# Optimization experiments

Measured on AMD Instinct MI355X. Metric: run time of the kernel, lower is better.

## Reference

```python
import jax, jax.numpy as jnp
import numpy as np

N = 100000      # num_nodes
E = 1_600_000   # edges (avg degree 16)
D_IN = 128
D_H = 128
D_OUT = 128


def setup_inputs() -> dict:
    key = jax.random.key(0)
    ks = jax.random.split(key, 11)
    x = jax.random.normal(ks[0], (N, D_IN), dtype=jnp.float32)
    edge_index = jax.random.randint(ks[1], (2, E), 0, N, dtype=jnp.int32)
    s_in = 1.0 / np.sqrt(D_IN)
    s_h = 1.0 / np.sqrt(D_H)
    return {
        "x": x,
        "edge_index": edge_index,
        "W_neigh1": jax.random.uniform(ks[2], (D_H, D_IN), jnp.float32, -s_in, s_in),
        "b_neigh1": jax.random.uniform(ks[3], (D_H,), jnp.float32, -s_in, s_in),
        "W_self1": jax.random.uniform(ks[4], (D_H, D_IN), jnp.float32, -s_in, s_in),
        "b_self1": jax.random.uniform(ks[5], (D_H,), jnp.float32, -s_in, s_in),
        "W_neigh2": jax.random.uniform(ks[6], (D_OUT, D_H), jnp.float32, -s_h, s_h),
        "b_neigh2": jax.random.uniform(ks[7], (D_OUT,), jnp.float32, -s_h, s_h),
        "W_self2": jax.random.uniform(ks[8], (D_OUT, D_H), jnp.float32, -s_h, s_h),
        "b_self2": jax.random.uniform(ks[9], (D_OUT,), jnp.float32, -s_h, s_h),
    }


def reference(x, edge_index, W_neigh1, b_neigh1, W_self1, b_self1,
              W_neigh2, b_neigh2, W_self2, b_self2):
    src, dst = edge_index[0], edge_index[1]
    n = x.shape[0]
    # row-normalized adjacency: deg over dst (row index), clamped to >= 1
    deg = jax.ops.segment_sum(jnp.ones(src.shape[0], x.dtype), dst, num_segments=n)
    inv_deg = 1.0 / jnp.maximum(deg, 1.0)  # [N]

    def agg(h):  # mean aggregation: (A_rownorm @ h)
        return jax.ops.segment_sum(h[src], dst, num_segments=n) * inv_deg[:, None]

    h1 = agg(x) @ W_neigh1.T + b_neigh1 + x @ W_self1.T + b_self1
    h1 = jax.nn.relu(h1)
    # dropout omitted (eval-mode / deterministic reference)
    h2 = agg(h1) @ W_neigh2.T + b_neigh2 + h1 @ W_self2.T + b_self2
    return h2
```

## Files before the change

### kernel.cpp

```cpp
#include <hip/hip_runtime.h>
#include <hip/hip_bf16.h>


typedef __attribute__((ext_vector_type(8))) short short8;
typedef __attribute__((ext_vector_type(4))) float float4_;

#define NBMAX 512

__device__ __forceinline__ unsigned short f2bf(float f) {
    unsigned int u = __float_as_uint(f);
    unsigned int r = (u + 0x7FFFu + ((u >> 16) & 1u)) >> 16;
    return (unsigned short)r;
}

__global__ __launch_bounds__(256) void bucket_count(const int* __restrict__ dst, int E, int NB,
                                                    int* __restrict__ bucketCnt) {
    __shared__ int h[NBMAX];
    int tid = threadIdx.x;
    for (int b = tid; b < NB; b += 256) h[b] = 0;
    __syncthreads();
    int base = blockIdx.x * 4096;
    for (int i = 0; i < 16; i++) {
        int e = base + i * 256 + tid;
        if (e < E) atomicAdd(&h[dst[e] >> 8], 1);
    }
    __syncthreads();
    for (int b = tid; b < NB; b += 256)
        if (h[b]) atomicAdd(&bucketCnt[b], h[b]);
}

__global__ __launch_bounds__(512) void bucket_scan(const int* __restrict__ bucketCnt, int NB,
                                                   int* __restrict__ bucketOffs,
                                                   int* __restrict__ bucketCur) {
    __shared__ int sd[512];
    int t = threadIdx.x;
    int v = (t < NB) ? bucketCnt[t] : 0;
    sd[t] = v;
    __syncthreads();
    for (int off = 1; off < 512; off <<= 1) {
        int x = sd[t];
        int y = (t >= off) ? sd[t - off] : 0;
        __syncthreads();
        sd[t] = x + y;
        __syncthreads();
    }
    int excl = sd[t] - v;
    if (t <= NB) bucketOffs[t] = excl;
    if (t < NB) bucketCur[t] = excl;
}

__global__ __launch_bounds__(256) void partition_wprep(
    const int* __restrict__ src, const int* __restrict__ dst, int E, int NB, int partBlocks,
    int* __restrict__ bucketCur, unsigned int* __restrict__ bucketBuf,
    const float* __restrict__ Wn1, const float* __restrict__ Ws1,
    const float* __restrict__ bn1, const float* __restrict__ bs1,
    const float* __restrict__ Wn2, const float* __restrict__ Ws2,
    const float* __restrict__ bn2, const float* __restrict__ bs2,
    unsigned short* __restrict__ Bpre, float* __restrict__ biasPre) {
    int tid = threadIdx.x;
    if ((int)blockIdx.x >= partBlocks) {
        int wb = blockIdx.x - partBlocks;
        int l = wb >> 4;
        const float* Wn = l ? Wn2 : Wn1;
        const float* Ws = l ? Ws2 : Ws1;
        int fi = (wb & 15) * 256 + tid;
        int kt = fi >> 9;
        int nt = (fi >> 6) & 7;
        int lane = fi & 63;
        int o = nt * 16 + (lane & 15);
        int k = kt * 32 + (lane >> 4) * 8;
        const float* srcp = (k < 128) ? (Wn + o * 128 + k) : (Ws + o * 128 + (k - 128));
        short8 v;
#pragma unroll
        for (int j = 0; j < 8; j++) v[j] = (short)f2bf(srcp[j]);
        ((short8*)(Bpre + (size_t)l * 32768))[fi] = v;
        if ((wb & 15) == 0 && tid < 128) {
            const float* bn = l ? bn2 : bn1;
            const float* bs = l ? bs2 : bs1;
            biasPre[l * 128 + tid] = bn[tid] + bs[tid];
        }
        return;
    }
    __shared__ int cnt[NBMAX];
    __shared__ int base[NBMAX];
    for (int b = tid; b < NB; b += 256) cnt[b] = 0;
    __syncthreads();
    int eb = blockIdx.x * 4096;
    unsigned int pk[16];
    int bk[16], rk[16];
    for (int i = 0; i < 16; i++) {
        int e = eb + i * 256 + tid;
        if (e < E) {
            int d = dst[e];
            bk[i] = d >> 8;
            pk[i] = (unsigned)src[e] | ((unsigned)(d & 255) << 24);
            rk[i] = atomicAdd(&cnt[bk[i]], 1);
        } else {
            bk[i] = -1;
        }
    }
    __syncthreads();
    for (int b = tid; b < NB; b += 256)
        base[b] = cnt[b] ? atomicAdd(&bucketCur[b], cnt[b]) : 0;
    __syncthreads();
    for (int i = 0; i < 16; i++)
        if (bk[i] >= 0) bucketBuf[base[bk[i]] + rk[i]] = pk[i];
}

__global__ __launch_bounds__(256) void csrbuild_cvt(
    const unsigned int* __restrict__ bucketBuf, const int* __restrict__ bucketOffs,
    int N, int NB, int* __restrict__ deg, int* __restrict__ offs, int* __restrict__ sortedSrc,
    const float* __restrict__ xin, unsigned int* __restrict__ xb, int n2) {
    int tid = threadIdx.x;
    if ((int)blockIdx.x >= NB) {
        int cb = blockIdx.x - NB;
        int base = cb * 2048 + tid;
        if (xb) {
#pragma unroll
            for (int i = 0; i < 8; i++) {
                int t = base + i * 256;
                if (t < n2) {
                    float2 v = ((const float2*)xin)[t];
                    xb[t] = (unsigned)f2bf(v.x) | ((unsigned)f2bf(v.y) << 16);
                }
            }
        }
        return;
    }
    __shared__ int h[256];
    __shared__ int sc[256];
    __shared__ int cur[256];
    int b = blockIdx.x;
    int n0 = b << 8;
    int bo = bucketOffs[b];
    int cnt = bucketOffs[b + 1] - bo;
    h[tid] = 0;
    __syncthreads();
    for (int i = tid; i < cnt; i += 256) atomicAdd(&h[bucketBuf[bo + i] >> 24], 1);
    __syncthreads();
    int v = h[tid];
    sc[tid] = v;
    __syncthreads();
    for (int off = 1; off < 256; off <<= 1) {
        int x = sc[tid];
        int y = (tid >= off) ? sc[tid - off] : 0;
        __syncthreads();
        sc[tid] = x + y;
        __syncthreads();
    }
    int excl = sc[tid] - v;
    cur[tid] = bo + excl;
    int n = n0 + tid;
    if (n < N) {
        deg[n] = v;
        offs[n] = bo + excl;
    }
    __syncthreads();
    for (int i = tid; i < cnt; i += 256) {
        unsigned int pv = bucketBuf[bo + i];
        int pos = atomicAdd(&cur[pv >> 24], 1);
        sortedSrc[pos] = (int)(pv & 0xFFFFFFu);
    }
}

__global__ __launch_bounds__(256) void agg_bf16_kernel(
    const unsigned int* __restrict__ srcFeats,
    const int* __restrict__ deg, const int* __restrict__ offs,
    const int* __restrict__ sortedSrc,
    unsigned int* __restrict__ dst, int Nn) {
    int wave = threadIdx.x >> 6, lane = threadIdx.x & 63;
    int n = blockIdx.x * 4 + wave;
    if (n >= Nn) return;
    int d = deg[n], st = offs[n];
    float a0 = 0.f, a1 = 0.f;
    int j = 0;
    for (; j + 16 <= d; j += 16) {
        unsigned int uu[16];
#pragma unroll
        for (int u = 0; u < 16; u++) {
            int s = __builtin_amdgcn_readfirstlane(sortedSrc[st + j + u]);
            uu[u] = (srcFeats + (size_t)s * 64)[lane];
        }
#pragma unroll
        for (int u = 0; u < 16; u++) {
            a0 += __uint_as_float(uu[u] << 16);
            a1 += __uint_as_float(uu[u] & 0xFFFF0000u);
        }
    }
    for (; j + 8 <= d; j += 8) {
        unsigned int uu[8];
#pragma unroll
        for (int u = 0; u < 8; u++) {
            int s = __builtin_amdgcn_readfirstlane(sortedSrc[st + j + u]);
            uu[u] = (srcFeats + (size_t)s * 64)[lane];
        }
#pragma unroll
        for (int u = 0; u < 8; u++) {
            a0 += __uint_as_float(uu[u] << 16);
            a1 += __uint_as_float(uu[u] & 0xFFFF0000u);
        }
    }
    for (; j < d; j++) {
        int s = __builtin_amdgcn_readfirstlane(sortedSrc[st + j]);
        unsigned int u = (srcFeats + (size_t)s * 64)[lane];
        a0 += __uint_as_float(u << 16);
        a1 += __uint_as_float(u & 0xFFFF0000u);
    }
    float inv = 1.0f / (float)max(d, 1);
    dst[(size_t)n * 64 + lane] = (unsigned)f2bf(a0 * inv) | ((unsigned)f2bf(a1 * inv) << 16);
}

__global__ __launch_bounds__(256) void agg_f32_kernel(
    const float* __restrict__ srcFeats,
    const int* __restrict__ deg, const int* __restrict__ offs,
    const int* __restrict__ sortedSrc,
    unsigned int* __restrict__ dst, int Nn) {
    int wave = threadIdx.x >> 6, lane = threadIdx.x & 63;
    int n = blockIdx.x * 4 + wave;
    if (n >= Nn) return;
    int d = deg[n], st = offs[n];
    float a0 = 0.f, a1 = 0.f;
    int j = 0;
    for (; j + 8 <= d; j += 8) {
        float2 v[8];
#pragma unroll
        for (int u = 0; u < 8; u++) {
            int s = __builtin_amdgcn_readfirstlane(sortedSrc[st + j + u]);
            v[u] = ((const float2*)(srcFeats + (size_t)s * 128))[lane];
        }
#pragma unroll
        for (int u = 0; u < 8; u++) {
            a0 += v[u].x;
            a1 += v[u].y;
        }
    }
    for (; j < d; j++) {
        int s = __builtin_amdgcn_readfirstlane(sortedSrc[st + j]);
        float2 v = ((const float2*)(srcFeats + (size_t)s * 128))[lane];
        a0 += v.x;
        a1 += v.y;
    }
    float inv = 1.0f / (float)max(d, 1);
    dst[(size_t)n * 64 + lane] = (unsigned)f2bf(a0 * inv) | ((unsigned)f2bf(a1 * inv) << 16);
}

__global__ __launch_bounds__(256) void gemm_kernel(
    const unsigned short* __restrict__ Aagg, const void* Aself,
    const unsigned short* __restrict__ Bpre, const float* __restrict__ biasPre,
    void* Out, int relu, int selfF32, int outBf16, int Nrows) {
    __shared__ unsigned short ldsB[8 * 8 * 64 * 8];
    __shared__ float biasS[128];
    int tid = threadIdx.x;

#pragma unroll
    for (int i = 0; i < 16; i++) {
        int fi = tid + 256 * i;
        ((short8*)ldsB)[fi] = ((const short8*)Bpre)[fi];
    }
    if (tid < 128) biasS[tid] = biasPre[tid];
    __syncthreads();

    int wave = tid >> 6, lane = tid & 63;
    int quad = lane >> 4, mr = lane & 15;
    int rowBase = blockIdx.x * 128 + wave * 32;

    float4_ acc[2][8];
    float4_ z = {0.f, 0.f, 0.f, 0.f};
    for (int mt = 0; mt < 2; mt++)
        for (int nt = 0; nt < 8; nt++) acc[mt][nt] = z;

    for (int kt = 0; kt < 8; kt++) {
        int kk = (kt & 3) * 32 + quad * 8;
        short8 a[2];
        for (int mt = 0; mt < 2; mt++) {
            int row = rowBase + mt * 16 + mr;
            if (row >= Nrows) row = Nrows - 1;
            if (kt < 4) {
                a[mt] = *(const short8*)(Aagg + (size_t)row * 128 + kk);
            } else if (selfF32) {
                const float* p = (const float*)Aself + (size_t)row * 128 + kk;
                float4_ f0 = *(const float4_*)p;
                float4_ f1 = *(const float4_*)(p + 4);
                short8 t;
#pragma unroll
                for (int j = 0; j < 4; j++) {
                    t[j] = (short)f2bf(f0[j]);
                    t[4 + j] = (short)f2bf(f1[j]);
                }
                a[mt] = t;
            } else {
                a[mt] = *(const short8*)((const unsigned short*)Aself + (size_t)row * 128 + kk);
            }
        }
        for (int nt = 0; nt < 8; nt++) {
            short8 b = *(const short8*)(ldsB + ((size_t)(kt * 8 + nt) * 64 + lane) * 8);
            acc[0][nt] = __builtin_amdgcn_mfma_f32_16x16x32_bf16(a[0], b, acc[0][nt], 0, 0, 0);
            acc[1][nt] = __builtin_amdgcn_mfma_f32_16x16x32_bf16(a[1], b, acc[1][nt], 0, 0, 0);
        }
    }

    for (int mt = 0; mt < 2; mt++) {
        for (int nt = 0; nt < 8; nt++) {
            int col = nt * 16 + mr;
            float bv = biasS[col];
            for (int r = 0; r < 4; r++) {
                int row = rowBase + mt * 16 + quad * 4 + r;
                if (row < Nrows) {
                    float v = acc[mt][nt][r] + bv;
                    if (relu) v = fmaxf(v, 0.f);
                    if (outBf16)
                        ((unsigned short*)Out)[(size_t)row * 128 + col] = f2bf(v);
                    else
                        ((float*)Out)[(size_t)row * 128 + col] = v;
                }
            }
        }
    }
}

extern "C" void kernel_launch(void* const* d_in, const int* in_sizes, int n_in,
                              void* d_out, int out_size, void* d_ws, size_t ws_size,
                              hipStream_t stream) {
    const float* x = (const float*)d_in[0];
    const int* ei = (const int*)d_in[1];
    const float* Wn1 = (const float*)d_in[2];
    const float* bn1 = (const float*)d_in[3];
    const float* Ws1 = (const float*)d_in[4];
    const float* bs1 = (const float*)d_in[5];
    const float* Wn2 = (const float*)d_in[6];
    const float* bn2 = (const float*)d_in[7];
    const float* Ws2 = (const float*)d_in[8];
    const float* bs2 = (const float*)d_in[9];

    const int N = in_sizes[0] / 128;
    const int E = in_sizes[1] / 2;
    const int* srcI = ei;
    const int* dstI = ei + E;
    const int NB = (N + 255) >> 8;

    char* ws = (char*)d_ws;
    size_t off = 0;
    auto alloc = [&](size_t bytes) -> void* {
        void* p = ws + off;
        off += (bytes + 255) & ~(size_t)255;
        return p;
    };
    int* deg = (int*)alloc((size_t)N * 4);
    int* offs = (int*)alloc((size_t)N * 4);
    int* bucketCnt = (int*)alloc((NBMAX + 1) * 4);
    int* bucketOffs = (int*)alloc((NBMAX + 1) * 4);
    int* bucketCur = (int*)alloc((NBMAX + 1) * 4);
    unsigned short* Bpre = (unsigned short*)alloc(2 * 32768 * 2);
    float* biasPre = (float*)alloc(2 * 128 * 4);
    int* sortedSrc = (int*)alloc((size_t)E * 4);
    unsigned short* Aagg = (unsigned short*)alloc((size_t)N * 128 * 2);
    size_t baseNeed = off;
    size_t bf16Buf = ((size_t)N * 128 * 2 + 255) & ~(size_t)255;
    bool bigWs = (ws_size >= baseNeed + 2 * bf16Buf);
    unsigned int* xb = nullptr;
    unsigned short* h1b = nullptr;
    if (bigWs) {
        xb = (unsigned int*)alloc((size_t)N * 128 * 2);
        h1b = (unsigned short*)alloc((size_t)N * 128 * 2);
    }
    unsigned int* bucketBuf = (unsigned int*)Aagg;

    int ebBlocks = (E + 4095) / 4096;
    int n2 = N * 64;
    int cvtBlocks = bigWs ? (n2 + 2047) / 2048 : 0;
    hipMemsetAsync(bucketCnt, 0, (size_t)NB * 4, stream);
    bucket_count<<<ebBlocks, 256, 0, stream>>>(dstI, E, NB, bucketCnt);
    bucket_scan<<<1, 512, 0, stream>>>(bucketCnt, NB, bucketOffs, bucketCur);
    partition_wprep<<<ebBlocks + 32, 256, 0, stream>>>(
        srcI, dstI, E, NB, ebBlocks, bucketCur, bucketBuf,
        Wn1, Ws1, bn1, bs1, Wn2, Ws2, bn2, bs2, Bpre, biasPre);
    csrbuild_cvt<<<NB + cvtBlocks, 256, 0, stream>>>(bucketBuf, bucketOffs, N, NB, deg, offs,
                                                     sortedSrc, x, xb, n2);

    int aggBlocks = (N + 3) / 4;
    int gemmBlocks = (N + 127) / 128;

    if (bigWs) {
        agg_bf16_kernel<<<aggBlocks, 256, 0, stream>>>(xb, deg, offs, sortedSrc,
                                                       (unsigned int*)Aagg, N);
        gemm_kernel<<<gemmBlocks, 256, 0, stream>>>(Aagg, xb, Bpre, biasPre, h1b, 1, 0, 1, N);
        agg_bf16_kernel<<<aggBlocks, 256, 0, stream>>>((const unsigned int*)h1b, deg, offs,
                                                       sortedSrc, (unsigned int*)Aagg, N);
        gemm_kernel<<<gemmBlocks, 256, 0, stream>>>(Aagg, h1b, Bpre + 32768, biasPre + 128,
                                                    d_out, 0, 0, 0, N);
    } else {
        float* h1 = (float*)d_out;
        agg_f32_kernel<<<aggBlocks, 256, 0, stream>>>(x, deg, offs, sortedSrc,
                                                      (unsigned int*)Aagg, N);
        gemm_kernel<<<gemmBlocks, 256, 0, stream>>>(Aagg, x, Bpre, biasPre, h1, 1, 1, 0, N);
        agg_f32_kernel<<<aggBlocks, 256, 0, stream>>>(h1, deg, offs, sortedSrc,
                                                      (unsigned int*)Aagg, N);
        gemm_kernel<<<gemmBlocks, 256, 0, stream>>>(Aagg, h1, Bpre + 32768, biasPre + 128,
                                                    d_out, 0, 1, 0, N);
    }
}
```

Baseline: 350.7 us.

## Build CSR with global-atomic degree count and grid-barrier scan

Replaces the two-level bucket partition CSR build (bucket count, bucket scan, partition, per-bucket local sort) with a per-node degree count via global atomics, a single-kernel two-level prefix scan synchronized by a software grid barrier, and a direct atomic scatter of src indices into sortedSrc. The x-to-bf16 conversion moves into the degree-count kernel. This removes one kernel launch and the intermediate bucket buffer pass, in exchange for many contended global atomics on random destinations and a spin-wait grid barrier that assumes all ~391 blocks are co-resident.

After: 504.8 us. +44.0%, slower.

```diff
diff --git a/kernel.cpp b/kernel.cpp
--- a/kernel.cpp
+++ b/kernel.cpp
@@ -13,45 +13,105 @@
     return (unsigned short)r;
 }
 
-__global__ __launch_bounds__(256) void bucket_count(const int* __restrict__ dst, int E, int NB,
-                                                    int* __restrict__ bucketCnt) {
-    __shared__ int h[NBMAX];
+__device__ __forceinline__ void gbar(int* bar, int id, int G) {
+    __syncthreads();
+    if (threadIdx.x == 0) {
+        __threadfence();
+        atomicAdd(&bar[id], 1);
+        while (atomicAdd(&bar[id], 0) < G) __builtin_amdgcn_s_sleep(16);
+        __threadfence();
+    }
+    __syncthreads();
+}
+
+__global__ __launch_bounds__(256) void deg_cvt(
+    const int* __restrict__ dst, int E, int cntBlocks, int* __restrict__ deg,
+    const float* __restrict__ xin, unsigned int* __restrict__ xb, int n2) {
     int tid = threadIdx.x;
-    for (int b = tid; b < NB; b += 256) h[b] = 0;
-    __syncthreads();
+    if ((int)blockIdx.x >= cntBlocks) {
+        int cb = blockIdx.x - cntBlocks;
+        int base = cb * 2048 + tid;
+        if (xb) {
+#pragma unroll
+            for (int i = 0; i < 8; i++) {
+                int t = base + i * 256;
+                if (t < n2) {
+                    float2 v = ((const float2*)xin)[t];
+                    xb[t] = (unsigned)f2bf(v.x) | ((unsigned)f2bf(v.y) << 16);
+                }
+            }
+        }
+        return;
+    }
     int base = blockIdx.x * 4096;
     for (int i = 0; i < 16; i++) {
         int e = base + i * 256 + tid;
-        if (e < E) atomicAdd(&h[dst[e] >> 8], 1);
-    }
+        if (e < E) atomicAdd(&deg[dst[e]], 1);
+    }
+}
+
+__global__ __launch_bounds__(256) void scan_offs(
+    const int* __restrict__ deg, int N, int NBv, int G,
+    int* __restrict__ partialS, int* __restrict__ gBase,
+    int* __restrict__ offs, int* __restrict__ cur, int* __restrict__ bar) {
+    __shared__ int sc[256];
+    int b = blockIdx.x, tid = threadIdx.x;
+    int n = b * 256 + tid;
+    int v = (n < N) ? deg[n] : 0;
+    sc[tid] = v;
     __syncthreads();
-    for (int b = tid; b < NB; b += 256)
-        if (h[b]) atomicAdd(&bucketCnt[b], h[b]);
-}
-
-__global__ __launch_bounds__(512) void bucket_scan(const int* __restrict__ bucketCnt, int NB,
-                                                   int* __restrict__ bucketOffs,
-                                                   int* __restrict__ bucketCur) {
-    __shared__ int sd[512];
-    int t = threadIdx.x;
-    int v = (t < NB) ? bucketCnt[t] : 0;
-    sd[t] = v;
-    __syncthreads();
-    for (int off = 1; off < 512; off <<= 1) {
-        int x = sd[t];
-        int y = (t >= off) ? sd[t - off] : 0;
-        __syncthreads();
-        sd[t] = x + y;
-        __syncthreads();
-    }
-    int excl = sd[t] - v;
-    if (t <= NB) bucketOffs[t] = excl;
-    if (t < NB) bucketCur[t] = excl;
-}
-
-__global__ __launch_bounds__(256) void partition_wprep(
-    const int* __restrict__ src, const int* __restrict__ dst, int E, int NB, int partBlocks,
-    int* __restrict__ bucketCur, unsigned int* __restrict__ bucketBuf,
+    for (int off = 1; off < 256; off <<= 1) {
+        int x = sc[tid];
+        int y = (tid >= off) ? sc[tid - off] : 0;
+        __syncthreads();
+        sc[tid] = x + y;
+        __syncthreads();
+    }
+    int excl = sc[tid] - v;
+    if (tid == 0) partialS[b] = sc[255];
+    gbar(bar, 0, G);
+    if (b == 0) {
+        int v0 = (tid < NBv) ? partialS[tid] : 0;
+        int j = 256 + tid;
+        int v1 = (j < NBv) ? partialS[j] : 0;
+        sc[tid] = v0;
+        __syncthreads();
+        for (int off = 1; off < 256; off <<= 1) {
+            int x = sc[tid];
+            int y = (tid >= off) ? sc[tid - off] : 0;
+            __syncthreads();
+            sc[tid] = x + y;
+            __syncthreads();
+        }
+        int inc0 = sc[tid];
+        int tot0 = sc[255];
+        __syncthreads();
+        sc[tid] = v1;
+        __syncthreads();
+        for (int off = 1; off < 256; off <<= 1) {
+            int x = sc[tid];
+            int y = (tid >= off) ? sc[tid - off] : 0;
+            __syncthreads();
+            sc[tid] = x + y;
+            __syncthreads();
+        }
+        int inc1 = sc[tid];
+        __syncthreads();
+        gBase[tid] = inc0 - v0;
+        gBase[j] = tot0 + inc1 - v1;
+    }
+    gbar(bar, 1, G);
+    int base = gBase[b];
+    if (n < N) {
+        int o = base + excl;
+        offs[n] = o;
+        cur[n] = o;
+    }
+}
+
+__global__ __launch_bounds__(256) void scatter_wprep(
+    const int* __restrict__ src, const int* __restrict__ dst, int E, int partBlocks,
+    int* __restrict__ cur, int* __restrict__ sortedSrc,
     const float* __restrict__ Wn1, const float* __restrict__ Ws1,
     const float* __restrict__ bn1, const float* __restrict__ bs1,
     const float* __restrict__ Wn2, const float* __restrict__ Ws2,
@@ -81,85 +141,14 @@
         }
         return;
     }
-    __shared__ int cnt[NBMAX];
-    __shared__ int base[NBMAX];
-    for (int b = tid; b < NB; b += 256) cnt[b] = 0;
-    __syncthreads();
     int eb = blockIdx.x * 4096;
-    unsigned int pk[16];
-    int bk[16], rk[16];
     for (int i = 0; i < 16; i++) {
         int e = eb + i * 256 + tid;
         if (e < E) {
             int d = dst[e];
-            bk[i] = d >> 8;
-            pk[i] = (unsigned)src[e] | ((unsigned)(d & 255) << 24);
-            rk[i] = atomicAdd(&cnt[bk[i]], 1);
-        } else {
-            bk[i] = -1;
-        }
-    }
-    __syncthreads();
-    for (int b = tid; b < NB; b += 256)
-        base[b] = cnt[b] ? atomicAdd(&bucketCur[b], cnt[b]) : 0;
-    __syncthreads();
-    for (int i = 0; i < 16; i++)
-        if (bk[i] >= 0) bucketBuf[base[bk[i]] + rk[i]] = pk[i];
-}
-
-__global__ __launch_bounds__(256) void csrbuild_cvt(
-    const unsigned int* __restrict__ bucketBuf, const int* __restrict__ bucketOffs,
-    int N, int NB, int* __restrict__ deg, int* __restrict__ offs, int* __restrict__ sortedSrc,
-    const float* __restrict__ xin, unsigned int* __restrict__ xb, int n2) {
-    int tid = threadIdx.x;
-    if ((int)blockIdx.x >= NB) {
-        int cb = blockIdx.x - NB;
-        int base = cb * 2048 + tid;
-        if (xb) {
-#pragma unroll
-            for (int i = 0; i < 8; i++) {
-                int t = base + i * 256;
-                if (t < n2) {
-                    float2 v = ((const float2*)xin)[t];
-                    xb[t] = (unsigned)f2bf(v.x) | ((unsigned)f2bf(v.y) << 16);
-                }
-            }
-        }
-        return;
-    }
-    __shared__ int h[256];
-    __shared__ int sc[256];
-    __shared__ int cur[256];
-    int b = blockIdx.x;
-    int n0 = b << 8;
-    int bo = bucketOffs[b];
-    int cnt = bucketOffs[b + 1] - bo;
-    h[tid] = 0;
-    __syncthreads();
-    for (int i = tid; i < cnt; i += 256) atomicAdd(&h[bucketBuf[bo + i] >> 24], 1);
-    __syncthreads();
-    int v = h[tid];
-    sc[tid] = v;
-    __syncthreads();
-    for (int off = 1; off < 256; off <<= 1) {
-        int x = sc[tid];
-        int y = (tid >= off) ? sc[tid - off] : 0;
-        __syncthreads();
-        sc[tid] = x + y;
-        __syncthreads();
-    }
-    int excl = sc[tid] - v;
-    cur[tid] = bo + excl;
-    int n = n0 + tid;
-    if (n < N) {
-        deg[n] = v;
-        offs[n] = bo + excl;
-    }
-    __syncthreads();
-    for (int i = tid; i < cnt; i += 256) {
-        unsigned int pv = bucketBuf[bo + i];
-        int pos = atomicAdd(&cur[pv >> 24], 1);
-        sortedSrc[pos] = (int)(pv & 0xFFFFFFu);
+            int pos = atomicAdd(&cur[d], 1);
+            sortedSrc[pos] = src[e];
+        }
     }
 }
 
@@ -336,7 +325,8 @@
     const int E = in_sizes[1] / 2;
     const int* srcI = ei;
     const int* dstI = ei + E;
-    const int NB = (N + 255) >> 8;
+    const int ebBlocks = (E + 4095) / 4096;
+    const int NBv = (N + 255) >> 8;
 
     char* ws = (char*)d_ws;
     size_t off = 0;
@@ -346,10 +336,12 @@
         return p;
     };
     int* deg = (int*)alloc((size_t)N * 4);
+    int* bar = (int*)alloc(64);
+    size_t zeroBytes = off;
     int* offs = (int*)alloc((size_t)N * 4);
-    int* bucketCnt = (int*)alloc((NBMAX + 1) * 4);
-    int* bucketOffs = (int*)alloc((NBMAX + 1) * 4);
-    int* bucketCur = (int*)alloc((NBMAX + 1) * 4);
+    int* cur = (int*)alloc((size_t)N * 4);
+    int* partialS = (int*)alloc(NBMAX * 4);
+    int* gBase = (int*)alloc(NBMAX * 4);
     unsigned short* Bpre = (unsigned short*)alloc(2 * 32768 * 2);
     float* biasPre = (float*)alloc(2 * 128 * 4);
     int* sortedSrc = (int*)alloc((size_t)E * 4);
@@ -363,19 +355,15 @@
         xb = (unsigned int*)alloc((size_t)N * 128 * 2);
         h1b = (unsigned short*)alloc((size_t)N * 128 * 2);
     }
-    unsigned int* bucketBuf = (unsigned int*)Aagg;
-
-    int ebBlocks = (E + 4095) / 4096;
+
     int n2 = N * 64;
     int cvtBlocks = bigWs ? (n2 + 2047) / 2048 : 0;
-    hipMemsetAsync(bucketCnt, 0, (size_t)NB * 4, stream);
-    bucket_count<<<ebBlocks, 256, 0, stream>>>(dstI, E, NB, bucketCnt);
-    bucket_scan<<<1, 512, 0, stream>>>(bucketCnt, NB, bucketOffs, bucketCur);
-    partition_wprep<<<ebBlocks + 32, 256, 0, stream>>>(
-        srcI, dstI, E, NB, ebBlocks, bucketCur, bucketBuf,
+    hipMemsetAsync(deg, 0, zeroBytes, stream);
+    deg_cvt<<<ebBlocks + cvtBlocks, 256, 0, stream>>>(dstI, E, ebBlocks, deg, x, xb, n2);
+    scan_offs<<<NBv, 256, 0, stream>>>(deg, N, NBv, NBv, partialS, gBase, offs, cur, bar);
+    scatter_wprep<<<ebBlocks + 32, 256, 0, stream>>>(
+        srcI, dstI, E, ebBlocks, cur, sortedSrc,
         Wn1, Ws1, bn1, bs1, Wn2, Ws2, bn2, bs2, Bpre, biasPre);
-    csrbuild_cvt<<<NB + cvtBlocks, 256, 0, stream>>>(bucketBuf, bucketOffs, N, NB, deg, offs,
-                                                     sortedSrc, x, xb, n2);
 
     int aggBlocks = (N + 3) / 4;
     int gemmBlocks = (N + 127) / 128;
```
